# Kernel optimization log

Hardware: AMD Instinct MI355X
Metric: run time of the kernel (lower is better)

Reference implementation:

```python
import jax, jax.numpy as jnp
import numpy as np
import math

N_PATCH = 216   # 6^3 sliding patches of a 20^3 tensor
DIM = 125       # 5^3 flattened patch
HEADS = 8
HEAD_DIM = 64
NSIDE = 6
EPS_BN = 1e-5
EPS_NORM = 1e-12


def batchnorm_train(x, w, b):
    # x: [B, C, H, W]; training-mode BN: biased batch stats over (B, H, W)
    mean = jnp.mean(x, axis=(0, 2, 3), keepdims=True)
    var = jnp.mean((x - mean) ** 2, axis=(0, 2, 3), keepdims=True)
    xh = (x - mean) / jnp.sqrt(var + EPS_BN)
    return xh * w[None, :, None, None] + b[None, :, None, None]


def l2_normalize(x, axis):
    n = jnp.sqrt(jnp.sum(x * x, axis=axis, keepdims=True))
    return x / jnp.maximum(n, EPS_NORM)


def sparsemax_dim1(z):
    # z: [B, N, M]; sparsemax along axis=1
    n = z.shape[1]
    zs = -jnp.sort(-z, axis=1)                       # descending sort
    ks = jnp.arange(1, n + 1, dtype=z.dtype)[None, :, None]
    cs = jnp.cumsum(zs, axis=1)
    support = 1.0 + ks * zs > cs                     # support set indicator
    k_star = jnp.sum(support, axis=1, keepdims=True).astype(z.dtype)
    tau = (jnp.sum(jnp.where(support, zs, 0.0), axis=1, keepdims=True) - 1.0) / k_star
    return jnp.maximum(z - tau, 0.0)


def setup_inputs() -> dict:
    key = jax.random.key(0)
    ks = jax.random.split(key, 6)
    return {
        "patches": jax.random.normal(ks[0], (1, N_PATCH, 5, 5, 5), jnp.float32),
        "Wq": jax.random.normal(ks[1], (HEADS * HEAD_DIM, DIM), jnp.float32) * 0.05,
        "Wk": jax.random.normal(ks[2], (HEADS * HEAD_DIM, DIM), jnp.float32) * 0.05,
        "bn_weight": jnp.ones((HEADS,), jnp.float32),
        "bn_bias": jnp.zeros((HEADS,), jnp.float32),
        "W1": jax.random.normal(ks[3], (20, 72), jnp.float32) * 0.05,
        "W2": jax.random.normal(ks[4], (20, 72), jnp.float32) * 0.05,
        "W3": jax.random.normal(ks[5], (20, 72), jnp.float32) * 0.05,
    }


def reference(patches, Wq, Wk, bn_weight, bn_bias, W1, W2, W3):
    B = 1
    x = patches.reshape(B, N_PATCH, DIM)                       # [1,216,125]
    q = x @ Wq.T                                               # [1,216,512]
    k = x @ Wk.T
    Q = q.reshape(B, N_PATCH, HEADS, HEAD_DIM).transpose(0, 2, 1, 3)  # [1,8,216,64]
    K = k.reshape(B, N_PATCH, HEADS, HEAD_DIM).transpose(0, 2, 1, 3)
    Q = l2_normalize(batchnorm_train(Q, bn_weight, bn_bias), axis=3)
    K = l2_normalize(batchnorm_train(K, bn_weight, bn_bias), axis=3)
    scores = jnp.einsum('bhnd,bhmd->bhnm', Q, K) / math.sqrt(DIM)     # [1,8,216,216]
    scores = scores.transpose(0, 2, 1, 3).reshape(B, N_PATCH, HEADS * N_PATCH)
    att = sparsemax_dim1(scores)                               # [1,216,1728] (dropout=eval)
    # [2,2,2,6,6,6,6,6,6] -> permute -> [1,72,72,72]
    x4 = att.reshape(2, 2, 2, NSIDE, NSIDE, NSIDE, NSIDE, NSIDE, NSIDE)
    x4 = x4.transpose(0, 3, 6, 1, 4, 7, 2, 5, 8).reshape(1, 72, 72, 72)
    # TCL: multi-mode contraction with factors [20,72]
    x5 = jnp.einsum('bijk,ai,cj,dk->bacd', x4, W1, W2, W3)     # [1,20,20,20]
    return jnp.tanh(x5), att
```

## Files before the change

kernel.cpp:

```cpp
#include <hip/hip_runtime.h>
#include <hip/hip_bf16.h>
#include <float.h>

#define N_PATCH 216
#define DIM 125
#define HEADS 8
#define HEAD_DIM 64
#define QK 512
#define NH (HEADS*N_PATCH)


__global__ __launch_bounds__(256) void k_wt(const float* __restrict__ Wq,
        const float* __restrict__ Wk, float* __restrict__ Wt) {
    __shared__ float lds[64*DIM];
    const int bid = blockIdx.x;
    const int t = threadIdx.x;
    const float* src = (bid < 8) ? Wq : Wk;
    const int rbase = (bid & 7)*64*DIM;
    for (int idx = t; idx < 64*DIM; idx += 256)
        lds[idx] = src[rbase + idx];
    __syncthreads();
    const int lane = t & 63, ii = t >> 6;
    const int c0 = bid*64;
    for (int i = ii; i < DIM; i += 4)
        Wt[i*1024 + c0 + lane] = lds[lane*DIM + i];
}

__global__ __launch_bounds__(512) void k_qk(const float* __restrict__ x,
        const float* __restrict__ Wt, float* __restrict__ q, float* __restrict__ k) {
    __shared__ float xs[DIM];
    const int n = blockIdx.x, t = threadIdx.x;
    if (t < DIM) xs[t] = x[n*DIM + t];
    __syncthreads();
    const float2* Wt2 = (const float2*)Wt;
    float2 acc = {0.f, 0.f};
    #pragma unroll 5
    for (int i = 0; i < DIM; ++i) {
        float2 w = Wt2[i*512 + t];
        float xv = xs[i];
        acc.x = fmaf(xv, w.x, acc.x);
        acc.y = fmaf(xv, w.y, acc.y);
    }
    int c = 2*t;
    if (c < QK) *(float2*)(q + n*QK + c) = acc;
    else        *(float2*)(k + n*QK + (c - QK)) = acc;
}

__global__ __launch_bounds__(256) void k_stats(const float* __restrict__ q,
        const float* __restrict__ k, float* __restrict__ stats) {
    const int bid = blockIdx.x;
    const int t = threadIdx.x;
    const float* src = (bid < 8) ? q : k;
    const int h = bid & 7;
    float s = 0.f, ss = 0.f;
    for (int idx = t; idx < N_PATCH*HEAD_DIM; idx += 256) {
        int n = idx >> 6, d = idx & 63;
        float v = src[n*QK + h*HEAD_DIM + d];
        s += v; ss += v*v;
    }
    for (int off = 32; off; off >>= 1) {
        s  += __shfl_down(s,  off, 64);
        ss += __shfl_down(ss, off, 64);
    }
    __shared__ float rs[4], rss[4];
    int wv = t >> 6, lane = t & 63;
    if (lane == 0) { rs[wv] = s; rss[wv] = ss; }
    __syncthreads();
    if (t == 0) {
        float S = rs[0]+rs[1]+rs[2]+rs[3];
        float SS = rss[0]+rss[1]+rss[2]+rss[3];
        const float invN = 1.0f/13824.0f;
        float mean = S*invN;
        float var  = SS*invN - mean*mean;
        stats[bid*2]   = mean;
        stats[bid*2+1] = var;
    }
}

__global__ __launch_bounds__(256) void k_norm(const float* __restrict__ q,
        const float* __restrict__ k, const float* __restrict__ stats,
        const float* __restrict__ bnw, const float* __restrict__ bnb,
        float* __restrict__ Qt, float* __restrict__ Kn) {
    int gw = blockIdx.x*4 + (threadIdx.x >> 6);
    int lane = threadIdx.x & 63;
    int isK = (gw >= NH) ? 1 : 0;
    int r = isK ? gw - NH : gw;
    int h = r / N_PATCH, n = r % N_PATCH;
    const float* src = isK ? k : q;
    int sb = (isK*8 + h)*2;
    float mean = stats[sb], var = stats[sb+1];
    float inv = 1.0f / sqrtf(var + 1e-5f);
    float w = bnw[h], b = bnb[h];
    float v = src[n*QK + h*HEAD_DIM + lane];
    float xh = (v - mean)*inv*w + b;
    float sq = xh*xh;
    for (int off = 32; off; off >>= 1) sq += __shfl_xor(sq, off, 64);
    float nrm = fmaxf(sqrtf(sq), 1e-12f);
    float o = xh / nrm;
    if (isK) Kn[(h*N_PATCH + n)*HEAD_DIM + lane] = o;
    else     Qt[h*HEAD_DIM*N_PATCH + lane*N_PATCH + n] = o;
}

__global__ __launch_bounds__(256) void k_sparsemax(const float* __restrict__ Qt,
        const float* __restrict__ Kn, float* __restrict__ att, float* __restrict__ x4) {
    const int c = blockIdx.x;
    const int h = c / N_PATCH, m = c % N_PATCH;
    const int tid = threadIdx.x;
    __shared__ float ks[HEAD_DIM];
    __shared__ float sz[256];
    __shared__ float wtot[4], rk[4], rssum[4];
    if (tid < HEAD_DIM) ks[tid] = Kn[(h*N_PATCH+m)*HEAD_DIM + tid];
    __syncthreads();
    float z = 0.f;
    const float* qt = Qt + h*HEAD_DIM*N_PATCH;
    if (tid < N_PATCH) {
        #pragma unroll 8
        for (int d = 0; d < HEAD_DIM; ++d) z += qt[d*N_PATCH + tid]*ks[d];
        z *= 0.08944271909999159f;
    }
    sz[tid] = (tid < N_PATCH) ? z : -FLT_MAX;
    __syncthreads();
    for (int kk = 2; kk <= 256; kk <<= 1) {
        for (int j = kk >> 1; j > 0; j >>= 1) {
            int ixj = tid ^ j;
            if (ixj > tid) {
                float a = sz[tid], bb = sz[ixj];
                bool desc = ((tid & kk) == 0);
                if (desc ? (a < bb) : (a > bb)) { sz[tid] = bb; sz[ixj] = a; }
            }
            __syncthreads();
        }
    }
    float sv = sz[tid];
    int lane = tid & 63, wv = tid >> 6;
    float cs = sv;
    for (int off = 1; off < 64; off <<= 1) {
        float t = __shfl_up(cs, off, 64);
        if (lane >= off) cs += t;
    }
    if (lane == 63) wtot[wv] = cs;
    __syncthreads();
    for (int p = 0; p < wv; ++p) cs += wtot[p];
    float supp = 0.f, ssel = 0.f;
    if (tid < N_PATCH && (1.0f + (float)(tid+1)*sv > cs)) { supp = 1.f; ssel = sv; }
    float s1 = supp, s2 = ssel;
    for (int off = 32; off; off >>= 1) {
        s1 += __shfl_xor(s1, off, 64);
        s2 += __shfl_xor(s2, off, 64);
    }
    if (lane == 0) { rk[wv] = s1; rssum[wv] = s2; }
    __syncthreads();
    float kstar = rk[0]+rk[1]+rk[2]+rk[3];
    float ssum  = rssum[0]+rssum[1]+rssum[2]+rssum[3];
    float tau = (ssum - 1.0f)/kstar;
    if (tid < N_PATCH) {
        float a = fmaxf(z - tau, 0.0f);
        att[tid*NH + c] = a;
        int nh2 = tid / 27;
        int d0 = nh2 >> 2, d1 = (nh2 >> 1) & 1, d2 = nh2 & 1;
        int r = (tid % 27)*NH + c;
        int d3 = r / 7776; r -= d3*7776;
        int d4 = r / 1296; r -= d4*1296;
        int d5 = r / 216;  r -= d5*216;
        int d6 = r / 36;   r -= d6*36;
        int d7 = r / 6;
        int d8 = r - d7*6;
        int ii  = d0*36 + d3*6 + d6;
        int jj  = d1*36 + d4*6 + d7;
        int kk2 = d2*36 + d5*6 + d8;
        x4[(ii*72 + jj)*72 + kk2] = a;
    }
}

__global__ __launch_bounds__(256) void k_tcl1(const float* __restrict__ W1,
        const float* __restrict__ x4, float* __restrict__ t1) {
    int o = blockIdx.x*256 + threadIdx.x;
    int a = o / 5184, jk = o % 5184;
    float acc = 0.f;
    #pragma unroll 8
    for (int i = 0; i < 72; ++i) acc += W1[a*72+i]*x4[i*5184 + jk];
    t1[o] = acc;
}

__global__ __launch_bounds__(256) void k_tcl2(const float* __restrict__ W2,
        const float* __restrict__ t1, float* __restrict__ t2) {
    int o = blockIdx.x*256 + threadIdx.x;
    if (o >= 28800) return;
    int a = o / 1440, rem = o % 1440;
    int cc = rem / 72, kk = rem % 72;
    float acc = 0.f;
    #pragma unroll 8
    for (int j = 0; j < 72; ++j) acc += W2[cc*72+j]*t1[a*5184 + j*72 + kk];
    t2[o] = acc;
}

__global__ __launch_bounds__(256) void k_tcl3(const float* __restrict__ W3,
        const float* __restrict__ t2, float* __restrict__ out0) {
    int o = blockIdx.x*256 + threadIdx.x;
    if (o >= 8000) return;
    int a = o / 400, rem = o % 400;
    int cc = rem / 20, dd = rem % 20;
    float acc = 0.f;
    #pragma unroll 8
    for (int k = 0; k < 72; ++k) acc += W3[dd*72+k]*t2[(a*20+cc)*72 + k];
    out0[o] = tanhf(acc);
}

extern "C" void kernel_launch(void* const* d_in, const int* in_sizes, int n_in,
                              void* d_out, int out_size, void* d_ws, size_t ws_size,
                              hipStream_t stream) {
    const float* patches = (const float*)d_in[0];
    const float* Wq = (const float*)d_in[1];
    const float* Wk = (const float*)d_in[2];
    const float* bnw = (const float*)d_in[3];
    const float* bnb = (const float*)d_in[4];
    const float* W1 = (const float*)d_in[5];
    const float* W2 = (const float*)d_in[6];
    const float* W3 = (const float*)d_in[7];
    float* out = (float*)d_out;
    float* ws = (float*)d_ws;

    float* Wt    = ws;
    float* q     = ws + 128000;
    float* k     = ws + 238592;
    float* stats = ws + 349184;
    float* Qt    = ws + 349216;
    float* Kn    = ws + 459808;
    float* x4    = ws + 570400;
    float* t1    = ws + 943648;
    float* t2    = ws + 1047328;

    float* out0 = out;
    float* att  = out + 8000;

    hipLaunchKernelGGL(k_wt,        dim3(16),   dim3(256), 0, stream, Wq, Wk, Wt);
    hipLaunchKernelGGL(k_qk,        dim3(216),  dim3(512), 0, stream, patches, Wt, q, k);
    hipLaunchKernelGGL(k_stats,     dim3(16),   dim3(256), 0, stream, q, k, stats);
    hipLaunchKernelGGL(k_norm,      dim3(864),  dim3(256), 0, stream, q, k, stats, bnw, bnb, Qt, Kn);
    hipLaunchKernelGGL(k_sparsemax, dim3(1728), dim3(256), 0, stream, Qt, Kn, att, x4);
    hipLaunchKernelGGL(k_tcl1,      dim3(405),  dim3(256), 0, stream, W1, x4, t1);
    hipLaunchKernelGGL(k_tcl2,      dim3(113),  dim3(256), 0, stream, W2, t1, t2);
    hipLaunchKernelGGL(k_tcl3,      dim3(32),   dim3(256), 0, stream, W3, t2, out0);
}
```

Measured before the change: 135.3 us.

## Replace bitonic-sort sparsemax with per-wave Newton threshold; fuse BN stats and TCL stages

Sparsemax now uses one wavefront per column and finds tau with a Newton-style iteration built on wave-shuffle reductions, instead of a 256-thread block doing a bitonic sort in LDS with many __syncthreads. BatchNorm statistics are accumulated with atomics inside the QK projection kernel, with stats zeroed in the weight-transpose kernel, and the normalization kernel derives mean and variance from the raw sums. The second and third TCL contractions are fused into one kernel that keeps intermediates in LDS. Together these cut several launches and remove the heavy sort. The cost is an iterative threshold with a tolerance and a 48-iteration cap, and atomic summation order that is not deterministic.

```diff
diff --git a/kernel.cpp b/kernel.cpp
--- a/kernel.cpp
+++ b/kernel.cpp
@@ -11,10 +11,11 @@
 
 
 __global__ __launch_bounds__(256) void k_wt(const float* __restrict__ Wq,
-        const float* __restrict__ Wk, float* __restrict__ Wt) {
+        const float* __restrict__ Wk, float* __restrict__ Wt, float* __restrict__ stats) {
     __shared__ float lds[64*DIM];
     const int bid = blockIdx.x;
     const int t = threadIdx.x;
+    if (bid == 0 && t < 32) stats[t] = 0.f;
     const float* src = (bid < 8) ? Wq : Wk;
     const int rbase = (bid & 7)*64*DIM;
     for (int idx = t; idx < 64*DIM; idx += 256)
@@ -27,7 +28,8 @@
 }
 
 __global__ __launch_bounds__(512) void k_qk(const float* __restrict__ x,
-        const float* __restrict__ Wt, float* __restrict__ q, float* __restrict__ k) {
+        const float* __restrict__ Wt, float* __restrict__ q, float* __restrict__ k,
+        float* __restrict__ stats) {
     __shared__ float xs[DIM];
     const int n = blockIdx.x, t = threadIdx.x;
     if (t < DIM) xs[t] = x[n*DIM + t];
@@ -44,36 +46,18 @@
     int c = 2*t;
     if (c < QK) *(float2*)(q + n*QK + c) = acc;
     else        *(float2*)(k + n*QK + (c - QK)) = acc;
-}
-
-__global__ __launch_bounds__(256) void k_stats(const float* __restrict__ q,
-        const float* __restrict__ k, float* __restrict__ stats) {
-    const int bid = blockIdx.x;
-    const int t = threadIdx.x;
-    const float* src = (bid < 8) ? q : k;
-    const int h = bid & 7;
-    float s = 0.f, ss = 0.f;
-    for (int idx = t; idx < N_PATCH*HEAD_DIM; idx += 256) {
-        int n = idx >> 6, d = idx & 63;
-        float v = src[n*QK + h*HEAD_DIM + d];
-        s += v; ss += v*v;
-    }
-    for (int off = 32; off; off >>= 1) {
-        s  += __shfl_down(s,  off, 64);
-        ss += __shfl_down(ss, off, 64);
-    }
-    __shared__ float rs[4], rss[4];
-    int wv = t >> 6, lane = t & 63;
-    if (lane == 0) { rs[wv] = s; rss[wv] = ss; }
-    __syncthreads();
-    if (t == 0) {
-        float S = rs[0]+rs[1]+rs[2]+rs[3];
-        float SS = rss[0]+rss[1]+rss[2]+rss[3];
-        const float invN = 1.0f/13824.0f;
-        float mean = S*invN;
-        float var  = SS*invN - mean*mean;
-        stats[bid*2]   = mean;
-        stats[bid*2+1] = var;
+    float s  = acc.x + acc.y;
+    float ss = acc.x*acc.x + acc.y*acc.y;
+    #pragma unroll
+    for (int off = 16; off; off >>= 1) {
+        s  += __shfl_down(s,  off, 32);
+        ss += __shfl_down(ss, off, 32);
+    }
+    if ((t & 31) == 0) {
+        int isK = (c >= QK) ? 1 : 0;
+        int h = (c & (QK-1)) >> 6;
+        atomicAdd(&stats[(isK*8+h)*2],   s);
+        atomicAdd(&stats[(isK*8+h)*2+1], ss);
     }
 }
 
@@ -88,12 +72,15 @@
     int h = r / N_PATCH, n = r % N_PATCH;
     const float* src = isK ? k : q;
     int sb = (isK*8 + h)*2;
-    float mean = stats[sb], var = stats[sb+1];
+    const float invN = 1.0f/13824.0f;
+    float mean = stats[sb]*invN;
+    float var  = stats[sb+1]*invN - mean*mean;
     float inv = 1.0f / sqrtf(var + 1e-5f);
     float w = bnw[h], b = bnb[h];
     float v = src[n*QK + h*HEAD_DIM + lane];
     float xh = (v - mean)*inv*w + b;
     float sq = xh*xh;
+    #pragma unroll
     for (int off = 32; off; off >>= 1) sq += __shfl_xor(sq, off, 64);
     float nrm = fmaxf(sqrtf(sq), 1e-12f);
     float o = xh / nrm;
@@ -101,64 +88,55 @@
     else     Qt[h*HEAD_DIM*N_PATCH + lane*N_PATCH + n] = o;
 }
 
-__global__ __launch_bounds__(256) void k_sparsemax(const float* __restrict__ Qt,
+__global__ __launch_bounds__(256) void k_sparse(const float* __restrict__ Qt,
         const float* __restrict__ Kn, float* __restrict__ att, float* __restrict__ x4) {
-    const int c = blockIdx.x;
+    const int wv = threadIdx.x >> 6, lane = threadIdx.x & 63;
+    const int c = blockIdx.x*4 + wv;
     const int h = c / N_PATCH, m = c % N_PATCH;
-    const int tid = threadIdx.x;
-    __shared__ float ks[HEAD_DIM];
-    __shared__ float sz[256];
-    __shared__ float wtot[4], rk[4], rssum[4];
-    if (tid < HEAD_DIM) ks[tid] = Kn[(h*N_PATCH+m)*HEAD_DIM + tid];
-    __syncthreads();
-    float z = 0.f;
-    const float* qt = Qt + h*HEAD_DIM*N_PATCH;
-    if (tid < N_PATCH) {
-        #pragma unroll 8
-        for (int d = 0; d < HEAD_DIM; ++d) z += qt[d*N_PATCH + tid]*ks[d];
-        z *= 0.08944271909999159f;
-    }
-    sz[tid] = (tid < N_PATCH) ? z : -FLT_MAX;
-    __syncthreads();
-    for (int kk = 2; kk <= 256; kk <<= 1) {
-        for (int j = kk >> 1; j > 0; j >>= 1) {
-            int ixj = tid ^ j;
-            if (ixj > tid) {
-                float a = sz[tid], bb = sz[ixj];
-                bool desc = ((tid & kk) == 0);
-                if (desc ? (a < bb) : (a > bb)) { sz[tid] = bb; sz[ixj] = a; }
-            }
-            __syncthreads();
+    __shared__ float ks[4][HEAD_DIM];
+    ks[wv][lane] = Kn[(h*N_PATCH+m)*HEAD_DIM + lane];
+    __syncthreads();
+    const float* qh = Qt + h*HEAD_DIM*N_PATCH;
+    float z0=0.f, z1=0.f, z2=0.f, z3=0.f;
+    const bool v3 = (lane < N_PATCH - 192);
+    #pragma unroll 8
+    for (int d = 0; d < HEAD_DIM; ++d) {
+        float kd = ks[wv][d];
+        z0 = fmaf(qh[d*N_PATCH + lane],       kd, z0);
+        z1 = fmaf(qh[d*N_PATCH + 64 + lane],  kd, z1);
+        z2 = fmaf(qh[d*N_PATCH + 128 + lane], kd, z2);
+        if (v3) z3 = fmaf(qh[d*N_PATCH + 192 + lane], kd, z3);
+    }
+    const float scale = 0.08944271909999159f;
+    z0 *= scale; z1 *= scale; z2 *= scale; z3 *= scale;
+    float mx = fmaxf(fmaxf(z0, z1), fmaxf(z2, v3 ? z3 : -FLT_MAX));
+    #pragma unroll
+    for (int off = 32; off; off >>= 1) mx = fmaxf(mx, __shfl_xor(mx, off, 64));
+    float tau = mx - 1.0f;
+    for (int it = 0; it < 48; ++it) {
+        float g = fmaxf(z0-tau,0.f) + fmaxf(z1-tau,0.f) + fmaxf(z2-tau,0.f)
+                + (v3 ? fmaxf(z3-tau,0.f) : 0.f);
+        float cnt = (z0>tau ? 1.f:0.f) + (z1>tau ? 1.f:0.f) + (z2>tau ? 1.f:0.f)
+                  + ((v3 && z3>tau) ? 1.f:0.f);
+        #pragma unroll
+        for (int off = 32; off; off >>= 1) {
+            g   += __shfl_xor(g,   off, 64);
+            cnt += __shfl_xor(cnt, off, 64);
         }
-    }
-    float sv = sz[tid];
-    int lane = tid & 63, wv = tid >> 6;
-    float cs = sv;
-    for (int off = 1; off < 64; off <<= 1) {
-        float t = __shfl_up(cs, off, 64);
-        if (lane >= off) cs += t;
-    }
-    if (lane == 63) wtot[wv] = cs;
-    __syncthreads();
-    for (int p = 0; p < wv; ++p) cs += wtot[p];
-    float supp = 0.f, ssel = 0.f;
-    if (tid < N_PATCH && (1.0f + (float)(tid+1)*sv > cs)) { supp = 1.f; ssel = sv; }
-    float s1 = supp, s2 = ssel;
-    for (int off = 32; off; off >>= 1) {
-        s1 += __shfl_xor(s1, off, 64);
-        s2 += __shfl_xor(s2, off, 64);
-    }
-    if (lane == 0) { rk[wv] = s1; rssum[wv] = s2; }
-    __syncthreads();
-    float kstar = rk[0]+rk[1]+rk[2]+rk[3];
-    float ssum  = rssum[0]+rssum[1]+rssum[2]+rssum[3];
-    float tau = (ssum - 1.0f)/kstar;
-    if (tid < N_PATCH) {
-        float a = fmaxf(z - tau, 0.0f);
-        att[tid*NH + c] = a;
-        int nh2 = tid / 27;
+        g -= 1.0f;
+        if (g <= 1e-7f) break;
+        tau += g / cnt;
+    }
+    #pragma unroll
+    for (int j = 0; j < 4; ++j) {
+        int n = lane + 64*j;
+        if (n >= N_PATCH) break;
+        float zz = (j==0) ? z0 : (j==1) ? z1 : (j==2) ? z2 : z3;
+        float a = fmaxf(zz - tau, 0.f);
+        att[n*NH + c] = a;
+        int nh2 = n / 27;
         int d0 = nh2 >> 2, d1 = (nh2 >> 1) & 1, d2 = nh2 & 1;
-        int r = (tid % 27)*NH + c;
+        int r = (n % 27)*NH + c;
         int d3 = r / 7776; r -= d3*7776;
         int d4 = r / 1296; r -= d4*1296;
         int d5 = r / 216;  r -= d5*216;
@@ -182,28 +160,29 @@
     t1[o] = acc;
 }
 
-__global__ __launch_bounds__(256) void k_tcl2(const float* __restrict__ W2,
-        const float* __restrict__ t1, float* __restrict__ t2) {
-    int o = blockIdx.x*256 + threadIdx.x;
-    if (o >= 28800) return;
-    int a = o / 1440, rem = o % 1440;
-    int cc = rem / 72, kk = rem % 72;
-    float acc = 0.f;
-    #pragma unroll 8
-    for (int j = 0; j < 72; ++j) acc += W2[cc*72+j]*t1[a*5184 + j*72 + kk];
-    t2[o] = acc;
-}
-
-__global__ __launch_bounds__(256) void k_tcl3(const float* __restrict__ W3,
-        const float* __restrict__ t2, float* __restrict__ out0) {
-    int o = blockIdx.x*256 + threadIdx.x;
-    if (o >= 8000) return;
-    int a = o / 400, rem = o % 400;
-    int cc = rem / 20, dd = rem % 20;
-    float acc = 0.f;
-    #pragma unroll 8
-    for (int k = 0; k < 72; ++k) acc += W3[dd*72+k]*t2[(a*20+cc)*72 + k];
-    out0[o] = tanhf(acc);
+__global__ __launch_bounds__(512) void k_tcl23(const float* __restrict__ W2,
+        const float* __restrict__ W3, const float* __restrict__ t1,
+        float* __restrict__ out0) {
+    __shared__ float t1a[5184];
+    __shared__ float t2a[1440];
+    const int a = blockIdx.x, t = threadIdx.x;
+    for (int i = t; i < 5184; i += 512) t1a[i] = t1[a*5184 + i];
+    __syncthreads();
+    for (int idx = t; idx < 1440; idx += 512) {
+        int cc = idx / 72, kk = idx % 72;
+        float acc = 0.f;
+        #pragma unroll 8
+        for (int j = 0; j < 72; ++j) acc += W2[cc*72+j]*t1a[j*72 + kk];
+        t2a[idx] = acc;
+    }
+    __syncthreads();
+    if (t < 400) {
+        int cc = t / 20, dd = t % 20;
+        float acc = 0.f;
+        #pragma unroll 8
+        for (int kq = 0; kq < 72; ++kq) acc += W3[dd*72+kq]*t2a[cc*72 + kq];
+        out0[(a*20 + cc)*20 + dd] = tanhf(acc);
+    }
 }
 
 extern "C" void kernel_launch(void* const* d_in, const int* in_sizes, int n_in,
@@ -228,17 +207,14 @@
     float* Kn    = ws + 459808;
     float* x4    = ws + 570400;
     float* t1    = ws + 943648;
-    float* t2    = ws + 1047328;
 
     float* out0 = out;
     float* att  = out + 8000;
 
-    hipLaunchKernelGGL(k_wt,        dim3(16),   dim3(256), 0, stream, Wq, Wk, Wt);
-    hipLaunchKernelGGL(k_qk,        dim3(216),  dim3(512), 0, stream, patches, Wt, q, k);
-    hipLaunchKernelGGL(k_stats,     dim3(16),   dim3(256), 0, stream, q, k, stats);
-    hipLaunchKernelGGL(k_norm,      dim3(864),  dim3(256), 0, stream, q, k, stats, bnw, bnb, Qt, Kn);
-    hipLaunchKernelGGL(k_sparsemax, dim3(1728), dim3(256), 0, stream, Qt, Kn, att, x4);
-    hipLaunchKernelGGL(k_tcl1,      dim3(405),  dim3(256), 0, stream, W1, x4, t1);
-    hipLaunchKernelGGL(k_tcl2,      dim3(113),  dim3(256), 0, stream, W2, t1, t2);
-    hipLaunchKernelGGL(k_tcl3,      dim3(32),   dim3(256), 0, stream, W3, t2, out0);
-}
+    hipLaunchKernelGGL(k_wt,     dim3(16),   dim3(256), 0, stream, Wq, Wk, Wt, stats);
+    hipLaunchKernelGGL(k_qk,     dim3(216),  dim3(512), 0, stream, patches, Wt, q, k, stats);
+    hipLaunchKernelGGL(k_norm,   dim3(864),  dim3(256), 0, stream, q, k, stats, bnw, bnb, Qt, Kn);
+    hipLaunchKernelGGL(k_sparse, dim3(432),  dim3(256), 0, stream, Qt, Kn, att, x4);
+    hipLaunchKernelGGL(k_tcl1,   dim3(405),  dim3(256), 0, stream, W1, x4, t1);
+    hipLaunchKernelGGL(k_tcl23,  dim3(20),   dim3(512), 0, stream, W2, W3, t1, out0);
+}
```

Result: slower. 162.0 us (+19.7%).
